# Optimization experiments

Hardware: AMD Instinct MI355X
Metric: run time of the kernel (lower is better)

The kernel has to match this reference:

```python
import math
import jax, jax.numpy as jnp
import numpy as np

EPS = 1e-5

def _ln(x, g, b, axes):
    # LayerNormalization4D / 4DCF: mean/var (unbiased=False) over `axes`
    mu = x.mean(axis=axes, keepdims=True)
    var = ((x - mu) ** 2).mean(axis=axes, keepdims=True)
    return (x - mu) / jnp.sqrt(var + EPS) * g + b

def _prelu(x, a):
    return jnp.where(x >= 0, x, a * x)

def _unfold(x, ks, hs):
    # x: [N, C, Q] -> [N, L, C*ks]; patch layout (c, k) matches F.unfold
    N, C, Qd = x.shape
    L = (Qd - ks) // hs + 1
    idx = jnp.arange(L) * hs
    p = x[:, :, idx[:, None] + jnp.arange(ks)]  # [N, C, L, ks]
    return p.transpose(0, 2, 1, 3).reshape(N, L, C * ks)

def _lstm_dir(xs, Wi, Wh, bi, bh, H):
    # xs: [N, L, Cin]; torch gate order i, f, g, o
    xg = jnp.einsum('nlc,gc->nlg', xs, Wi) + bi + bh  # [N, L, 4H]
    def step(carry, gt):
        h, c = carry
        g = gt + h @ Wh.T
        i, f, gg, o = jnp.split(g, 4, axis=-1)
        c = jax.nn.sigmoid(f) * c + jax.nn.sigmoid(i) * jnp.tanh(gg)
        h = jax.nn.sigmoid(o) * jnp.tanh(c)
        return (h, c), h
    N = xs.shape[0]
    z = jnp.zeros((N, H), xs.dtype)
    _, hs = jax.lax.scan(step, (z, z), jnp.swapaxes(xg, 0, 1))
    return jnp.swapaxes(hs, 0, 1)

def _bilstm(x, wih, whh, bih, bhh):
    H = whh.shape[-1]
    f = _lstm_dir(x, wih[0], whh[0], bih[0], bhh[0], H)
    bk = _lstm_dir(x[:, ::-1], wih[1], whh[1], bih[1], bhh[1], H)[:, ::-1]
    return jnp.concatenate([f, bk], axis=-1)

def _convT1d(x, w, b):
    # x: [N, I, L]; w: [I, O, K] (torch ConvTranspose1d layout); stride 1
    K = w.shape[2]
    w2 = jnp.transpose(w, (1, 0, 2))[:, :, ::-1]
    y = jax.lax.conv_general_dilated(x, w2, (1,), [(K - 1, K - 1)],
                                     dimension_numbers=('NCH', 'OIH', 'NCH'))
    return y + b[None, :, None]

def _forward(x, mouth, intra_g, intra_b, intra_wih, intra_whh, intra_bih, intra_bhh,
             intra_lw, intra_lb, inter_g, inter_b, inter_wih, inter_whh, inter_bih,
             inter_bhh, inter_lw, inter_lb, qw, qb, qa, qg, qbe, kw, kb, ka, kg, kbe,
             vw, vb, va, vg, vbe, pw, pb, pa, pg, pbe):
    emb_ks, emb_hs = 4, 1
    B, C, oT, oQ = x.shape
    T = math.ceil((oT - emb_ks) / emb_hs) * emb_hs + emb_ks
    Qd = math.ceil((oQ - emb_ks) / emb_hs) * emb_hs + emb_ks
    x = jnp.pad(x, ((0, 0), (0, 0), (0, T - oT), (0, Qd - oQ)))
    inp = x
    # ---- intra (biLSTM along freq axis) ----
    h = _ln(inp, intra_g[None, :, None, None], intra_b[None, :, None, None], (1,))
    h = h.transpose(0, 2, 1, 3).reshape(B * T, C, Qd)
    h = _unfold(h, emb_ks, emb_hs)                          # [B*T, L, C*ks]
    h = _bilstm(h, intra_wih, intra_whh, intra_bih, intra_bhh)
    h = _convT1d(h.transpose(0, 2, 1), intra_lw, intra_lb)  # [B*T, C, Qd]
    intra = h.reshape(B, T, C, Qd).transpose(0, 2, 1, 3) + inp
    # ---- inter (biLSTM along time axis) ----
    h = _ln(intra, inter_g[None, :, None, None], inter_b[None, :, None, None], (1,))
    h = h.transpose(0, 3, 1, 2).reshape(B * Qd, C, T)
    h = _unfold(h, emb_ks, emb_hs)
    h = _bilstm(h, inter_wih, inter_whh, inter_bih, inter_bhh)
    h = _convT1d(h.transpose(0, 2, 1), inter_lw, inter_lb)  # [B*Qd, C, T]
    inter = h.reshape(B, Qd, C, T).transpose(0, 2, 3, 1) + intra
    inter = inter[..., :oT, :oQ]                             # [B, C, oT, oQ]
    # ---- multi-head full self-attention over time (conv1x1 QKV per head) ----
    NH = qw.shape[0]
    def qkv(w, b_, a_, g_, be_):
        y = jnp.einsum('bctf,hec->hbetf', inter, w) + b_[:, None, :, None, None]
        y = _prelu(y, a_[:, None, None, None, None])
        return _ln(y, g_[:, None, :, None, :], be_[:, None, :, None, :], (2, 4))
    Qh = qkv(qw, qb, qa, qg, qbe)   # [H, B, E, T, F]
    Kh = qkv(kw, kb, ka, kg, kbe)
    Vh = qkv(vw, vb, va, vg, vbe)   # [H, B, D, T, F]
    E = Qh.shape[2]; D = Vh.shape[2]; F = oQ
    q2 = Qh.transpose(0, 1, 3, 2, 4).reshape(NH, B, oT, E * F)
    k2 = Kh.transpose(0, 1, 3, 2, 4).reshape(NH, B, oT, E * F)
    v2 = Vh.transpose(0, 1, 3, 2, 4).reshape(NH, B, oT, D * F)
    scale = 1.0 / jnp.sqrt(jnp.asarray(E * F, x.dtype))
    attn = jax.nn.softmax(jnp.einsum('hbte,hbse->hbts', q2, k2) * scale, axis=-1)
    o = jnp.einsum('hbts,hbsd->hbtd', attn, v2).reshape(NH, B, oT, D, F)
    o = o.transpose(1, 0, 3, 2, 4).reshape(B, NH * D, oT, F)
    # ---- concat projection ----
    p = jnp.einsum('bctf,oc->botf', o, pw) + pb[None, :, None, None]
    p = _prelu(p, pa)
    p = _ln(p, pg[None, :, None, :], pbe[None, :, None, :], (1, 3))
    return p + inter

def setup_inputs() -> dict:
    key = jax.random.key(0)
    keys = iter(jax.random.split(key, 48))
    f32 = jnp.float32
    def nrm(shape, s=0.05):
        return jax.random.normal(next(keys), shape, f32) * s
    B, C, T, F = 2, 48, 512, 65
    K, H, NH, E = 4, 192, 4, 8
    Cin = C * K
    D = C // NH
    return {
        'x': jax.random.normal(next(keys), (B, C, T, F), f32),
        'mouth': jax.random.normal(next(keys), (B, 64), f32),
        'intra_g': jnp.ones((C,), f32), 'intra_b': jnp.zeros((C,), f32),
        'intra_wih': nrm((2, 4 * H, Cin)), 'intra_whh': nrm((2, 4 * H, H)),
        'intra_bih': nrm((2, 4 * H)), 'intra_bhh': nrm((2, 4 * H)),
        'intra_lw': nrm((2 * H, C, K)), 'intra_lb': nrm((C,)),
        'inter_g': jnp.ones((C,), f32), 'inter_b': jnp.zeros((C,), f32),
        'inter_wih': nrm((2, 4 * H, Cin)), 'inter_whh': nrm((2, 4 * H, H)),
        'inter_bih': nrm((2, 4 * H)), 'inter_bhh': nrm((2, 4 * H)),
        'inter_lw': nrm((2 * H, C, K)), 'inter_lb': nrm((C,)),
        'qw': nrm((NH, E, C)), 'qb': nrm((NH, E)), 'qa': 0.25 * jnp.ones((NH,), f32),
        'qg': jnp.ones((NH, E, F), f32), 'qbe': jnp.zeros((NH, E, F), f32),
        'kw': nrm((NH, E, C)), 'kb': nrm((NH, E)), 'ka': 0.25 * jnp.ones((NH,), f32),
        'kg': jnp.ones((NH, E, F), f32), 'kbe': jnp.zeros((NH, E, F), f32),
        'vw': nrm((NH, D, C)), 'vb': nrm((NH, D)), 'va': 0.25 * jnp.ones((NH,), f32),
        'vg': jnp.ones((NH, D, F), f32), 'vbe': jnp.zeros((NH, D, F), f32),
        'pw': nrm((C, C)), 'pb': nrm((C,)), 'pa': jnp.float32(0.25),
        'pg': jnp.ones((C, F), f32), 'pbe': jnp.zeros((C, F), f32),
    }

def reference(x, mouth, intra_g, intra_b, intra_wih, intra_whh, intra_bih, intra_bhh,
              intra_lw, intra_lb, inter_g, inter_b, inter_wih, inter_whh, inter_bih,
              inter_bhh, inter_lw, inter_lb, qw, qb, qa, qg, qbe, kw, kb, ka, kg, kbe,
              vw, vb, va, vg, vbe, pw, pb, pa, pg, pbe):
    return _forward(x, mouth, intra_g, intra_b, intra_wih, intra_whh, intra_bih,
                    intra_bhh, intra_lw, intra_lb, inter_g, inter_b, inter_wih,
                    inter_whh, inter_bih, inter_bhh, inter_lw, inter_lb, qw, qb, qa,
                    qg, qbe, kw, kb, ka, kg, kbe, vw, vb, va, vg, vbe, pw, pb, pa,
                    pg, pbe)
```

## Files before the change

### kernel.cpp

```cpp
#include <hip/hip_runtime.h>
#include <hip/hip_bf16.h>

typedef __bf16 bf16x8 __attribute__((ext_vector_type(8)));
typedef unsigned short u16x8 __attribute__((ext_vector_type(8)));
typedef float f32x4 __attribute__((ext_vector_type(4)));

#define DEV static __device__ __forceinline__

DEV unsigned short f2bf(float f){
  __hip_bfloat16 h = __float2bfloat16(f);
  return __builtin_bit_cast(unsigned short, h);
}
DEV float b2f(unsigned short u){
  return __bfloat162float(__builtin_bit_cast(__hip_bfloat16, u));
}
DEV float sig2(float xs){
  return __builtin_amdgcn_rcpf(1.0f + __builtin_amdgcn_exp2f(-xs));
}
DEV float tanh2s(float xs){
  return 1.0f - 2.0f*__builtin_amdgcn_rcpf(__builtin_amdgcn_exp2f(xs + xs) + 1.0f);
}
DEV float tanh_n(float x){
  return 1.0f - 2.0f*__builtin_amdgcn_rcpf(__builtin_amdgcn_exp2f(x * 2.885390082f) + 1.0f);
}
DEV void lds_barrier(){
  asm volatile("s_waitcnt lgkmcnt(0)\ns_barrier" ::: "memory");
}


__global__ void zero16(uint4* p, size_t n){
  size_t i = (size_t)blockIdx.x*blockDim.x + threadIdx.x;
  size_t st = (size_t)gridDim.x*blockDim.x;
  uint4 z = make_uint4(0u,0u,0u,0u);
  for (; i < n; i += st) p[i] = z;
}

__global__ void cast_bf(const float* __restrict__ s, unsigned short* __restrict__ d, int n, float scale){
  int i = blockIdx.x*256 + threadIdx.x;
  if (i < n) d[i] = f2bf(s[i]*scale);
}

__global__ void bias_comb(const float* __restrict__ a, const float* __restrict__ b,
                          float* __restrict__ d, int n, float scale){
  int i = blockIdx.x*256 + threadIdx.x;
  if (i < n) d[i] = (a[i] + b[i])*scale;
}

__global__ void lwt_build(const float* __restrict__ lw, unsigned short* __restrict__ lwt){
  int i = blockIdx.x*256 + threadIdx.x;
  if (i < 384*48*4){
    int m = i / 192; int rest = i - m*192; int c = rest >> 2; int k = rest & 3;
    lwt[(size_t)c*1536 + k*384 + m] = f2bf(lw[i]);
  }
}

__global__ __launch_bounds__(256) void ln_unf_intra(
    const float* __restrict__ in, const float* __restrict__ g,
    const float* __restrict__ be, unsigned short* __restrict__ unf)
{
  int bt = blockIdx.x; int b = bt >> 9, t = bt & 511;
  __shared__ float v[48][66];
  __shared__ float mu[65], rs[65];
  __shared__ float g_l[48], b_l[48];
  const float* base = in + (size_t)b*(48*512*65) + (size_t)t*65;
  for (int i = threadIdx.x; i < 48*65; i += 256){
    int c = i/65, q = i - c*65;
    v[c][q] = base[(size_t)c*(512*65) + q];
  }
  if (threadIdx.x < 48){ g_l[threadIdx.x] = g[threadIdx.x]; b_l[threadIdx.x] = be[threadIdx.x]; }
  __syncthreads();
  if (threadIdx.x < 65){
    int q = threadIdx.x; float s=0.f, s2=0.f;
    #pragma unroll
    for (int c = 0; c < 48; c++){ float x = v[c][q]; s += x; s2 += x*x; }
    float m = s*(1.0f/48.0f);
    mu[q] = m; rs[q] = rsqrtf(s2*(1.0f/48.0f) - m*m + 1e-5f);
  }
  __syncthreads();
  unsigned short* orow = unf + (size_t)(b*512 + t)*62*192;
  for (int i = threadIdx.x; i < 62*192; i += 256){
    int l = i/192, j = i - l*192;
    int c = j >> 2, kk = j & 3, q = l + kk;
    float y = (v[c][q]-mu[q])*rs[q]*g_l[c] + b_l[c];
    orow[i] = f2bf(y);
  }
}

__global__ __launch_bounds__(256) void ln_unf_inter(
    const float* __restrict__ in, const float* __restrict__ g,
    const float* __restrict__ be, unsigned short* __restrict__ unf)
{
  int q = blockIdx.x % 65, b = blockIdx.x / 65;
  __shared__ float v[48][132];
  __shared__ float mu[131], rs[131];
  __shared__ float g_l[48], b_l[48];
  if (threadIdx.x < 48){ g_l[threadIdx.x] = g[threadIdx.x]; b_l[threadIdx.x] = be[threadIdx.x]; }
  const float* base = in + (size_t)b*(48*512*65) + q;
  unsigned short* orow = unf + (size_t)(b*65 + q)*509*192;
  for (int t0 = 0; t0 < 512; t0 += 128){
    for (int i = threadIdx.x; i < 48*131; i += 256){
      int c = i/131, tt = i - c*131;
      int t = t0 + tt; t = t > 511 ? 511 : t;
      v[c][tt] = base[((size_t)c*512 + t)*65];
    }
    __syncthreads();
    if (threadIdx.x < 131){
      int tt = threadIdx.x; float s=0.f, s2=0.f;
      #pragma unroll
      for (int c = 0; c < 48; c++){ float x = v[c][tt]; s += x; s2 += x*x; }
      float m = s*(1.0f/48.0f);
      mu[tt] = m; rs[tt] = rsqrtf(s2*(1.0f/48.0f) - m*m + 1e-5f);
    }
    __syncthreads();
    for (int i = threadIdx.x; i < 128*192; i += 256){
      int ll = i/192, j = i - ll*192;
      int l = t0 + ll;
      if (l < 509){
        int c = j >> 2, kk = j & 3, tt = ll + kk;
        float y = (v[c][tt]-mu[tt])*rs[tt]*g_l[c] + b_l[c];
        orow[(size_t)l*192 + j] = f2bf(y);
      }
    }
    __syncthreads();
  }
}

__global__ __launch_bounds__(256) void gemm_xg(
    const unsigned short* __restrict__ unf, const unsigned short* __restrict__ wib,
    const float* __restrict__ bias, unsigned short* __restrict__ xg,
    int NSEQ, int TW, int win0, int L, int nvalid)
{
  const int d = blockIdx.z;
  const int lane = threadIdx.x & 63, wave = threadIdx.x >> 6;
  const int kg = lane >> 4, lr = lane & 15;
  const int nslb = TW >> 3;
  const int sb  = blockIdx.x / nslb;
  const int slb = blockIdx.x - sb*nslb;
  const int nbase = blockIdx.y*64;
  const unsigned short* Bp = wib + (size_t)d*768*192;

  const unsigned short* abase[2];
  #pragma unroll
  for (int mt = 0; mt < 2; mt++){
    int sl = slb*8 + wave*2 + mt;
    int s = win0 + sl;
    int l = d ? (L-1-s) : s;
    l = l < 0 ? 0 : (l > L-1 ? L-1 : l);
    int seq = sb*16 + lr;
    seq = seq < nvalid ? seq : nvalid-1;
    abase[mt] = unf + ((size_t)seq*L + l)*192;
  }

  f32x4 acc[2][4] = {};
  #pragma unroll
  for (int kt = 0; kt < 6; kt++){
    int k0 = kt*32 + kg*8;
    bf16x8 a0 = *(const bf16x8*)(abase[0] + k0);
    bf16x8 a1 = *(const bf16x8*)(abase[1] + k0);
    #pragma unroll
    for (int nt = 0; nt < 4; nt++){
      int n = nbase + nt*16 + lr;
      bf16x8 bfr = *(const bf16x8*)(Bp + (size_t)n*192 + k0);
      acc[0][nt] = __builtin_amdgcn_mfma_f32_16x16x32_bf16(a0, bfr, acc[0][nt], 0,0,0);
      acc[1][nt] = __builtin_amdgcn_mfma_f32_16x16x32_bf16(a1, bfr, acc[1][nt], 0,0,0);
    }
  }
  #pragma unroll
  for (int mt = 0; mt < 2; mt++){
    int sl = slb*8 + wave*2 + mt;
    size_t rowb = (((size_t)d*(NSEQ>>4) + sb)*TW + sl)*768;
    #pragma unroll
    for (int nt = 0; nt < 4; nt++){
      int n = nbase + nt*16 + lr;
      float bs = bias[d*768 + n];
      ushort4 pk;
      pk.x = f2bf(acc[mt][nt][0] + bs);
      pk.y = f2bf(acc[mt][nt][1] + bs);
      pk.z = f2bf(acc[mt][nt][2] + bs);
      pk.w = f2bf(acc[mt][nt][3] + bs);
      *(ushort4*)(xg + (rowb + n)*16 + kg*4) = pk;
    }
  }
}

__global__ __launch_bounds__(768, 3) void lstm_rec(
    const unsigned short* __restrict__ xg,
    const unsigned short* __restrict__ whb,
    unsigned short* __restrict__ hs,
    float* __restrict__ state,
    int NSEQ, int TW, int win0, int L, int Qrows, int nvalid, int steps)
{
  const int d = blockIdx.y;
  const int seq0 = blockIdx.x * 16;
  const int tid = threadIdx.x;
  const int lane = tid & 63, w = tid >> 6;
  const int kg = lane >> 4, lr = lane & 15;
  const int col = w*16 + lr;

  __shared__ unsigned short h_lds[2][16][200];

  bf16x8 whf[4][6];
  #pragma unroll
  for (int g = 0; g < 4; g++){
    const unsigned short* wrow = whb + ((size_t)d*768 + g*192 + col)*192;
    #pragma unroll
    for (int kt = 0; kt < 6; kt++)
      whf[g][kt] = *(const bf16x8*)(wrow + kt*32 + kg*8);
  }

  float c_reg[4];
  unsigned short* hsp[4];
  bool val[4];
  const int l0 = d ? (L-1-win0) : win0;
  const ptrdiff_t ldelta = d ? -384 : 384;
  #pragma unroll
  for (int r = 0; r < 4; r++){
    int m = kg*4 + r;
    const float* st = state + (((size_t)d*NSEQ + seq0 + m)*2)*192;
    h_lds[0][m][col] = f2bf(st[col]);
    c_reg[r] = st[192 + col];
    val[r] = (seq0 + m) < nvalid;
    hsp[r] = hs + ((size_t)(seq0+m)*Qrows + (l0+3))*384 + d*192 + col;
  }
  lds_barrier();

  const unsigned short* xq0 = xg + ((((size_t)d*(NSEQ>>4) + blockIdx.x)*TW)*768)*16
                              + ((size_t)col)*16 + kg*4;
  const size_t SSTR = (size_t)768*16;

  uint2 pfA[4], pfB[4];
  {
    const unsigned short* p1 = xq0 + (steps > 1 ? SSTR : 0);
    #pragma unroll
    for (int g = 0; g < 4; g++){
      pfA[g] = *(const uint2*)(xq0 + (size_t)g*(192*16));
      pfB[g] = *(const uint2*)(p1  + (size_t)g*(192*16));
    }
  }

  int cur = 0;
  auto do_step = [&](uint2 (&pf)[4], int ss){
    f32x4 acc[4];
    #pragma unroll
    for (int g = 0; g < 4; g++){
      unsigned int lo = pf[g].x, hi = pf[g].y;
      acc[g][0] = b2f((unsigned short)(lo & 0xffffu));
      acc[g][1] = b2f((unsigned short)(lo >> 16));
      acc[g][2] = b2f((unsigned short)(hi & 0xffffu));
      acc[g][3] = b2f((unsigned short)(hi >> 16));
    }
    int nss = ss + 2; nss = nss > steps-1 ? steps-1 : nss;
    const unsigned short* np = xq0 + (size_t)nss*SSTR;
    #pragma unroll
    for (int g = 0; g < 4; g++)
      pf[g] = *(const uint2*)(np + (size_t)g*(192*16));
    #pragma unroll
    for (int kt = 0; kt < 6; kt++){
      bf16x8 a = *(const bf16x8*)(&h_lds[cur][lr][kt*32 + kg*8]);
      #pragma unroll
      for (int g = 0; g < 4; g++)
        acc[g] = __builtin_amdgcn_mfma_f32_16x16x32_bf16(a, whf[g][kt], acc[g], 0,0,0);
    }
    #pragma unroll
    for (int r = 0; r < 4; r++){
      float gi = sig2(acc[0][r]);
      float gf = sig2(acc[1][r]);
      float gg = tanh2s(acc[2][r]);
      float go = sig2(acc[3][r]);
      float c = gf*c_reg[r] + gi*gg;
      c_reg[r] = c;
      float h = go*tanh_n(c);
      unsigned short hb = f2bf(h);
      h_lds[cur^1][kg*4 + r][col] = hb;
      if (val[r]) *hsp[r] = hb;
      hsp[r] += ldelta;
    }
    lds_barrier();
    cur ^= 1;
  };

  for (int ss = 0; ss < steps; ss += 2){
    do_step(pfA, ss);
    if (ss + 1 < steps) do_step(pfB, ss + 1);
  }

  #pragma unroll
  for (int r = 0; r < 4; r++){
    int m = kg*4 + r;
    float* st = state + (((size_t)d*NSEQ + seq0 + m)*2)*192;
    st[col] = b2f(h_lds[cur][m][col]);
    st[192 + col] = c_reg[r];
  }
}

__global__ __launch_bounds__(256) void gemm_convt(
    const unsigned short* __restrict__ hs, const unsigned short* __restrict__ lwt,
    const float* __restrict__ lb, const float* __restrict__ addsrc, float* __restrict__ dst,
    int Q, int ddiv, int sA, int sB, int nvalid)
{
  const int lane = threadIdx.x & 63, wave = threadIdx.x >> 6;
  const int kg = lane >> 4, lr = lane & 15;
  const int rowbase = blockIdx.x*128 + wave*32;

  int an[2], aq[2];
  #pragma unroll
  for (int mt = 0; mt < 2; mt++){
    int row = rowbase + mt*16 + lr;
    an[mt] = row / Q; aq[mt] = row - an[mt]*Q;
  }
  f32x4 acc[2][4] = {};
  for (int kt = 0; kt < 48; kt++){
    int k0 = kt*32 + kg*8;
    int tap = k0 / 384;
    int m0 = k0 - tap*384;
    bf16x8 a[2];
    #pragma unroll
    for (int mt = 0; mt < 2; mt++)
      a[mt] = *(const bf16x8*)(hs + ((size_t)an[mt]*(Q+3) + (aq[mt]+3-tap))*384 + m0);
    #pragma unroll
    for (int nt = 0; nt < 4; nt++){
      bf16x8 bfr = *(const bf16x8*)(lwt + (size_t)(nt*16+lr)*1536 + k0);
      acc[0][nt] = __builtin_amdgcn_mfma_f32_16x16x32_bf16(a[0], bfr, acc[0][nt], 0,0,0);
      acc[1][nt] = __builtin_amdgcn_mfma_f32_16x16x32_bf16(a[1], bfr, acc[1][nt], 0,0,0);
    }
  }
  #pragma unroll
  for (int mt = 0; mt < 2; mt++)
  #pragma unroll
  for (int nt = 0; nt < 4; nt++){
    int n = nt*16 + lr;
    if (n >= 48) continue;
    #pragma unroll
    for (int r = 0; r < 4; r++){
      int row = rowbase + mt*16 + kg*4 + r;
      int ns = row / Q, q = row - ns*Q;
      if (ns >= nvalid) continue;
      size_t off = (size_t)(ns/ddiv)*(48*512*65) + (size_t)n*(512*65)
                 + (size_t)(ns % ddiv)*sA + (size_t)q*sB;
      dst[off] = acc[mt][nt][r] + lb[n] + addsrc[off];
    }
  }
}

__global__ __launch_bounds__(256) void gemm_rm(
    const unsigned short* __restrict__ A, const unsigned short* __restrict__ B, float* __restrict__ C,
    int lda, int ldb, int ldc, int KT, int nmax, long long strA, long long strB, long long strC)
{
  const int z = blockIdx.z;
  A += (size_t)z * strA; B += (size_t)z * strB; C += (size_t)z * strC;
  const int lane = threadIdx.x & 63, wave = threadIdx.x >> 6;
  const int kg = lane >> 4, lr = lane & 15;
  const int rowbase = blockIdx.x*128 + wave*32;
  const int nbase = blockIdx.y*64;
  f32x4 acc[2][4] = {};
  for (int kt = 0; kt < KT; kt++){
    int k0 = kt*32 + kg*8;
    bf16x8 a0 = *(const bf16x8*)(A + (size_t)(rowbase+lr)*lda + k0);
    bf16x8 a1 = *(const bf16x8*)(A + (size_t)(rowbase+16+lr)*lda + k0);
    #pragma unroll
    for (int nt = 0; nt < 4; nt++){
      bf16x8 bfr = *(const bf16x8*)(B + (size_t)(nbase+nt*16+lr)*ldb + k0);
      acc[0][nt] = __builtin_amdgcn_mfma_f32_16x16x32_bf16(a0, bfr, acc[0][nt], 0,0,0);
      acc[1][nt] = __builtin_amdgcn_mfma_f32_16x16x32_bf16(a1, bfr, acc[1][nt], 0,0,0);
    }
  }
  #pragma unroll
  for (int mt = 0; mt < 2; mt++)
  #pragma unroll
  for (int nt = 0; nt < 4; nt++)
  #pragma unroll
  for (int r = 0; r < 4; r++){
    int n = nbase + nt*16 + lr;
    if (n < nmax){
      int row = rowbase + mt*16 + kg*4 + r;
      C[(size_t)row*ldc + n] = acc[mt][nt][r];
    }
  }
}

__global__ __launch_bounds__(256) void qkv_k(
    const float* __restrict__ inter, const float* __restrict__ w, const float* __restrict__ bias,
    const float* __restrict__ alpha, const float* __restrict__ gam, const float* __restrict__ bet,
    unsigned short* __restrict__ out, int E, int mode)
{
  int t = blockIdx.x; int hb = blockIdx.y; int h = hb >> 1, b = hb & 1;
  __shared__ float in_l[48][66];
  __shared__ float w_l[12][48];
  __shared__ float y_l[780];
  __shared__ float rs1[4], rs2[4];
  const float* base = inter + (size_t)b*(48*512*65) + (size_t)t*65;
  for (int i = threadIdx.x; i < 48*65; i += 256){
    int c = i/65, f = i - c*65;
    in_l[c][f] = base[(size_t)c*(512*65) + f];
  }
  for (int i = threadIdx.x; i < E*48; i += 256) w_l[i/48][i - (i/48)*48] = w[(size_t)h*E*48 + i];
  __syncthreads();
  int nel = E*65;
  float a = alpha[h];
  float ps = 0.f, pq = 0.f;
  for (int i = threadIdx.x; i < nel; i += 256){
    int e = i/65, f = i - e*65;
    float s = bias[h*E + e];
    #pragma unroll
    for (int c = 0; c < 48; c++) s += w_l[e][c]*in_l[c][f];
    s = s >= 0.f ? s : a*s;
    y_l[i] = s; ps += s; pq += s*s;
  }
  #pragma unroll
  for (int o = 32; o; o >>= 1){ ps += __shfl_xor(ps, o); pq += __shfl_xor(pq, o); }
  if ((threadIdx.x & 63) == 0){ rs1[threadIdx.x>>6] = ps; rs2[threadIdx.x>>6] = pq; }
  __syncthreads();
  ps = rs1[0]+rs1[1]+rs1[2]+rs1[3]; pq = rs2[0]+rs2[1]+rs2[2]+rs2[3];
  float inv = 1.0f/(float)nel;
  float m = ps*inv; float rstd = rsqrtf(pq*inv - m*m + 1e-5f);
  for (int i = threadIdx.x; i < nel; i += 256){
    int e = i/65, f = i - e*65;
    float v = (y_l[i]-m)*rstd*gam[(size_t)(h*E+e)*65 + f] + bet[(size_t)(h*E+e)*65 + f];
    if (mode < 2) out[((size_t)hb*512 + t)*544 + i] = f2bf(v);
    else          out[((size_t)hb*832 + i)*512 + t] = f2bf(v);
  }
}

__global__ __launch_bounds__(256) void softmax_k(const float* __restrict__ S, unsigned short* __restrict__ P){
  size_t row = (size_t)blockIdx.y*512 + blockIdx.x;
  const float* s = S + row*512;
  int tid = threadIdx.x;
  float v0 = s[tid], v1 = s[tid+256];
  float m = fmaxf(v0, v1);
  #pragma unroll
  for (int o = 32; o; o >>= 1) m = fmaxf(m, __shfl_xor(m, o));
  __shared__ float r4[4], q4[4];
  if ((tid & 63) == 0) r4[tid>>6] = m;
  __syncthreads();
  m = fmaxf(fmaxf(r4[0], r4[1]), fmaxf(r4[2], r4[3]));
  const float sc = 0.04385290096535146f;
  float e0 = __expf((v0-m)*sc), e1 = __expf((v1-m)*sc);
  float su = e0 + e1;
  #pragma unroll
  for (int o = 32; o; o >>= 1) su += __shfl_xor(su, o);
  if ((tid & 63) == 0) q4[tid>>6] = su;
  __syncthreads();
  su = q4[0]+q4[1]+q4[2]+q4[3];
  float inv = __builtin_amdgcn_rcpf(su);
  unsigned short* p = P + row*512;
  p[tid] = f2bf(e0*inv); p[tid+256] = f2bf(e1*inv);
}

__global__ __launch_bounds__(256) void pout_k(
    const float* __restrict__ o, const float* __restrict__ pw, const float* __restrict__ pb,
    const float* __restrict__ pa, const float* __restrict__ pg, const float* __restrict__ pbe,
    const float* __restrict__ inter, float* __restrict__ out)
{
  int bt = blockIdx.x; int b = bt >> 9, t = bt & 511;
  __shared__ float o_l[48][66];
  __shared__ float pw_l[48][48];
  __shared__ float p_l[3120];
  __shared__ float rs1[4], rs2[4];
  for (int i = threadIdx.x; i < 48*65; i += 256){
    int c = i/65, f = i - c*65; int h = c/12, dd = c - h*12;
    o_l[c][f] = o[((size_t)(h*2+b)*512 + t)*780 + dd*65 + f];
  }
  for (int i = threadIdx.x; i < 48*48; i += 256) pw_l[i/48][i - (i/48)*48] = pw[i];
  __syncthreads();
  float a = pa[0];
  float ps = 0.f, pq = 0.f;
  for (int i = threadIdx.x; i < 3120; i += 256){
    int oc = i/65, f = i - oc*65;
    float s = pb[oc];
    #pragma unroll
    for (int c = 0; c < 48; c++) s += pw_l[oc][c]*o_l[c][f];
    s = s >= 0.f ? s : a*s;
    p_l[i] = s; ps += s; pq += s*s;
  }
  #pragma unroll
  for (int o2 = 32; o2; o2 >>= 1){ ps += __shfl_xor(ps, o2); pq += __shfl_xor(pq, o2); }
  if ((threadIdx.x & 63) == 0){ rs1[threadIdx.x>>6] = ps; rs2[threadIdx.x>>6] = pq; }
  __syncthreads();
  ps = rs1[0]+rs1[1]+rs1[2]+rs1[3]; pq = rs2[0]+rs2[1]+rs2[2]+rs2[3];
  float m = ps*(1.0f/3120.0f); float rstd = rsqrtf(pq*(1.0f/3120.0f) - m*m + 1e-5f);
  for (int i = threadIdx.x; i < 3120; i += 256){
    int oc = i/65, f = i - oc*65;
    size_t off = ((size_t)(b*48+oc)*512 + t)*65 + f;
    out[off] = (p_l[i]-m)*rstd*pg[i] + pbe[i] + inter[off];
  }
}


extern "C" void kernel_launch(void* const* d_in, const int* in_sizes, int n_in,
                              void* d_out, int out_size, void* d_ws, size_t ws_size,
                              hipStream_t stream)
{
  const float* x         = (const float*)d_in[0];
  const float* intra_g   = (const float*)d_in[2];
  const float* intra_b   = (const float*)d_in[3];
  const float* intra_wih = (const float*)d_in[4];
  const float* intra_whh = (const float*)d_in[5];
  const float* intra_bih = (const float*)d_in[6];
  const float* intra_bhh = (const float*)d_in[7];
  const float* intra_lw  = (const float*)d_in[8];
  const float* intra_lb  = (const float*)d_in[9];
  const float* inter_g   = (const float*)d_in[10];
  const float* inter_b   = (const float*)d_in[11];
  const float* inter_wih = (const float*)d_in[12];
  const float* inter_whh = (const float*)d_in[13];
  const float* inter_bih = (const float*)d_in[14];
  const float* inter_bhh = (const float*)d_in[15];
  const float* inter_lw  = (const float*)d_in[16];
  const float* inter_lb  = (const float*)d_in[17];
  const float* qw  = (const float*)d_in[18];
  const float* qb  = (const float*)d_in[19];
  const float* qa  = (const float*)d_in[20];
  const float* qg  = (const float*)d_in[21];
  const float* qbe = (const float*)d_in[22];
  const float* kw  = (const float*)d_in[23];
  const float* kb  = (const float*)d_in[24];
  const float* ka  = (const float*)d_in[25];
  const float* kgm = (const float*)d_in[26];
  const float* kbe = (const float*)d_in[27];
  const float* vw  = (const float*)d_in[28];
  const float* vb  = (const float*)d_in[29];
  const float* va  = (const float*)d_in[30];
  const float* vg  = (const float*)d_in[31];
  const float* vbe = (const float*)d_in[32];
  const float* pw  = (const float*)d_in[33];
  const float* pb  = (const float*)d_in[34];
  const float* pa  = (const float*)d_in[35];
  const float* pgm = (const float*)d_in[36];
  const float* pbe = (const float*)d_in[37];

  char* ws = (char*)d_ws;
  constexpr size_t WIB_INTRA = 0;
  constexpr size_t WHB_INTRA = 589824;
  constexpr size_t WIB_INTER = 1179648;
  constexpr size_t WHB_INTER = 1769472;
  constexpr size_t LWT_INTRA = 2359296;
  constexpr size_t LWT_INTER = 2555904;
  constexpr size_t BIAS_INTRA = 2752512;
  constexpr size_t BIAS_INTER = 2758656;
  constexpr size_t UNF   = 2764800;
  constexpr size_t INTER = 2764800;
  constexpr size_t STATE = 28311552;
  constexpr size_t HS    = 31457280;
  constexpr size_t INTRA = 84934656;
  constexpr size_t XG    = 97714176;
  constexpr size_t Q2B   = XG;
  constexpr size_t K2B   = XG + 4456448;
  constexpr size_t V2T   = XG + 8912896;
  constexpr size_t SCORES= XG + 15728640;
  constexpr size_t ATTNB = XG + 24117248;
  constexpr size_t OBUF  = XG + 28311552;

  auto U16 = [&](size_t off){ return (unsigned short*)(ws + off); };
  auto F32 = [&](size_t off){ return (float*)(ws + off); };

  const float LOG2E = 1.4426950408889634f;

  zero16<<<512,256,0,stream>>>((uint4*)(ws+LWT_INTRA), 393216/16);
  cast_bf<<<1152,256,0,stream>>>(intra_wih, U16(WIB_INTRA), 294912, LOG2E);
  cast_bf<<<1152,256,0,stream>>>(intra_whh, U16(WHB_INTRA), 294912, LOG2E);
  cast_bf<<<1152,256,0,stream>>>(inter_wih, U16(WIB_INTER), 294912, LOG2E);
  cast_bf<<<1152,256,0,stream>>>(inter_whh, U16(WHB_INTER), 294912, LOG2E);
  bias_comb<<<6,256,0,stream>>>(intra_bih, intra_bhh, F32(BIAS_INTRA), 1536, LOG2E);
  bias_comb<<<6,256,0,stream>>>(inter_bih, inter_bhh, F32(BIAS_INTER), 1536, LOG2E);
  lwt_build<<<288,256,0,stream>>>(intra_lw, U16(LWT_INTRA));
  lwt_build<<<288,256,0,stream>>>(inter_lw, U16(LWT_INTER));

  ln_unf_intra<<<1024,256,0,stream>>>(x, intra_g, intra_b, U16(UNF));
  zero16<<<2048,256,0,stream>>>((uint4*)(ws+HS), 53477376/16);
  zero16<<<2048,256,0,stream>>>((uint4*)(ws+STATE), 3145728/16);
  for (int w = 0; w < 4; w++){
    int win0 = w*16;
    int steps = (62 - win0) < 16 ? (62 - win0) : 16;
    gemm_xg<<<dim3(128,12,2),256,0,stream>>>(U16(UNF), U16(WIB_INTRA), F32(BIAS_INTRA), U16(XG),
                                             1024, 16, win0, 62, 1024);
    lstm_rec<<<dim3(64,2),768,0,stream>>>(U16(XG), U16(WHB_INTRA), U16(HS), F32(STATE),
                                          1024, 16, win0, 62, 68, 1024, steps);
  }
  gemm_convt<<<dim3(520,1),256,0,stream>>>(U16(HS), U16(LWT_INTRA), intra_lb, x, F32(INTRA),
                                           65, 512, 65, 1, 1024);

  ln_unf_inter<<<130,256,0,stream>>>(F32(INTRA), inter_g, inter_b, U16(UNF));
  zero16<<<2048,256,0,stream>>>((uint4*)(ws+HS), 51417600/16);
  zero16<<<2048,256,0,stream>>>((uint4*)(ws+STATE), 3145728/16);
  for (int w = 0; w < 8; w++){
    int win0 = w*64;
    int steps = (509 - win0) < 64 ? (509 - win0) : 64;
    gemm_xg<<<dim3(72,12,2),256,0,stream>>>(U16(UNF), U16(WIB_INTER), F32(BIAS_INTER), U16(XG),
                                            144, 64, win0, 509, 130);
    lstm_rec<<<dim3(9,2),768,0,stream>>>(U16(XG), U16(WHB_INTER), U16(HS), F32(STATE),
                                         144, 64, win0, 509, 515, 130, steps);
  }
  gemm_convt<<<dim3(576,1),256,0,stream>>>(U16(HS), U16(LWT_INTER), inter_lb, F32(INTRA), F32(INTER),
                                           512, 65, 1, 65, 130);

  zero16<<<2048,256,0,stream>>>((uint4*)(ws+Q2B), 15728640/16);
  qkv_k<<<dim3(512,8),256,0,stream>>>(F32(INTER), qw, qb, qa, qg, qbe, U16(Q2B), 8, 0);
  qkv_k<<<dim3(512,8),256,0,stream>>>(F32(INTER), kw, kb, ka, kgm, kbe, U16(K2B), 8, 1);
  qkv_k<<<dim3(512,8),256,0,stream>>>(F32(INTER), vw, vb, va, vg, vbe, U16(V2T), 12, 2);
  gemm_rm<<<dim3(4,8,8),256,0,stream>>>(U16(Q2B), U16(K2B), F32(SCORES),
                                        544, 544, 512, 17, 512,
                                        (long long)512*544, (long long)512*544, (long long)512*512);
  softmax_k<<<dim3(512,8),256,0,stream>>>(F32(SCORES), U16(ATTNB));
  gemm_rm<<<dim3(4,13,8),256,0,stream>>>(U16(ATTNB), U16(V2T), F32(OBUF),
                                         512, 512, 780, 16, 780,
                                         (long long)512*512, (long long)832*512, (long long)512*780);
  pout_k<<<1024,256,0,stream>>>(F32(OBUF), pw, pb, pa, pgm, pbe, F32(INTER), (float*)d_out);
}
```

Before: 1.979 ms.

## Reorder unfold layout to tap-major and tile convT GEMM through LDS

Reorders the unfolded-input feature layout from (c,k) to (k,c) and permutes the input-projection weights to match, so the LN/unfold kernels can write vectorized 8-element bf16 chunks. The inter-path LN/unfold now runs one block per (b,t) row, scattering into up to four unfold rows, which gives far more blocks than the old per-q kernel. The convT GEMM is templated per mode, stages its overlapping hidden-state window in LDS for reuse across taps, and in intra mode writes float4 coalesced outputs through an LDS transpose. The costs are larger LDS use per block and many scattered small stores in the inter unfold.

New measurement: 1.960 ms. About the same (-1.0%).

```diff
diff --git a/kernel.cpp b/kernel.cpp
--- a/kernel.cpp
+++ b/kernel.cpp
@@ -38,6 +38,15 @@
 __global__ void cast_bf(const float* __restrict__ s, unsigned short* __restrict__ d, int n, float scale){
   int i = blockIdx.x*256 + threadIdx.x;
   if (i < n) d[i] = f2bf(s[i]*scale);
+}
+
+__global__ void cast_wi(const float* __restrict__ s, unsigned short* __restrict__ d, float scale){
+  int i = blockIdx.x*256 + threadIdx.x;
+  if (i < 294912){
+    int dn = i/192, k = i - dn*192;
+    int c = k >> 2, kk = k & 3;
+    d[(size_t)dn*192 + kk*48 + c] = f2bf(s[i]*scale);
+  }
 }
 
 __global__ void bias_comb(const float* __restrict__ a, const float* __restrict__ b,
@@ -78,11 +87,22 @@
   }
   __syncthreads();
   unsigned short* orow = unf + (size_t)(b*512 + t)*62*192;
-  for (int i = threadIdx.x; i < 62*192; i += 256){
-    int l = i/192, j = i - l*192;
-    int c = j >> 2, kk = j & 3, q = l + kk;
-    float y = (v[c][q]-mu[q])*rs[q]*g_l[c] + b_l[c];
-    orow[i] = f2bf(y);
+  for (int idx = threadIdx.x; idx < 62*24; idx += 256){
+    int l = idx/24, jg = idx - l*24;
+    int kk = jg/6, c0 = (jg - kk*6)*8;
+    int q = l + kk;
+    ushort4 p0, p1;
+    float mq = mu[q], rq = rs[q];
+    p0.x = f2bf((v[c0+0][q]-mq)*rq*g_l[c0+0] + b_l[c0+0]);
+    p0.y = f2bf((v[c0+1][q]-mq)*rq*g_l[c0+1] + b_l[c0+1]);
+    p0.z = f2bf((v[c0+2][q]-mq)*rq*g_l[c0+2] + b_l[c0+2]);
+    p0.w = f2bf((v[c0+3][q]-mq)*rq*g_l[c0+3] + b_l[c0+3]);
+    p1.x = f2bf((v[c0+4][q]-mq)*rq*g_l[c0+4] + b_l[c0+4]);
+    p1.y = f2bf((v[c0+5][q]-mq)*rq*g_l[c0+5] + b_l[c0+5]);
+    p1.z = f2bf((v[c0+6][q]-mq)*rq*g_l[c0+6] + b_l[c0+6]);
+    p1.w = f2bf((v[c0+7][q]-mq)*rq*g_l[c0+7] + b_l[c0+7]);
+    *(ushort4*)(orow + (size_t)l*192 + kk*48 + c0) = p0;
+    *(ushort4*)(orow + (size_t)l*192 + kk*48 + c0 + 4) = p1;
   }
 }
 
@@ -90,38 +110,44 @@
     const float* __restrict__ in, const float* __restrict__ g,
     const float* __restrict__ be, unsigned short* __restrict__ unf)
 {
-  int q = blockIdx.x % 65, b = blockIdx.x / 65;
-  __shared__ float v[48][132];
-  __shared__ float mu[131], rs[131];
+  int bt = blockIdx.x; int b = bt >> 9, t = bt & 511;
+  __shared__ float v[48][66];
+  __shared__ float mu[65], rs[65];
   __shared__ float g_l[48], b_l[48];
+  const float* base = in + (size_t)b*(48*512*65) + (size_t)t*65;
+  for (int i = threadIdx.x; i < 48*65; i += 256){
+    int c = i/65, q = i - c*65;
+    v[c][q] = base[(size_t)c*(512*65) + q];
+  }
   if (threadIdx.x < 48){ g_l[threadIdx.x] = g[threadIdx.x]; b_l[threadIdx.x] = be[threadIdx.x]; }
-  const float* base = in + (size_t)b*(48*512*65) + q;
-  unsigned short* orow = unf + (size_t)(b*65 + q)*509*192;
-  for (int t0 = 0; t0 < 512; t0 += 128){
-    for (int i = threadIdx.x; i < 48*131; i += 256){
-      int c = i/131, tt = i - c*131;
-      int t = t0 + tt; t = t > 511 ? 511 : t;
-      v[c][tt] = base[((size_t)c*512 + t)*65];
-    }
-    __syncthreads();
-    if (threadIdx.x < 131){
-      int tt = threadIdx.x; float s=0.f, s2=0.f;
-      #pragma unroll
-      for (int c = 0; c < 48; c++){ float x = v[c][tt]; s += x; s2 += x*x; }
-      float m = s*(1.0f/48.0f);
-      mu[tt] = m; rs[tt] = rsqrtf(s2*(1.0f/48.0f) - m*m + 1e-5f);
-    }
-    __syncthreads();
-    for (int i = threadIdx.x; i < 128*192; i += 256){
-      int ll = i/192, j = i - ll*192;
-      int l = t0 + ll;
-      if (l < 509){
-        int c = j >> 2, kk = j & 3, tt = ll + kk;
-        float y = (v[c][tt]-mu[tt])*rs[tt]*g_l[c] + b_l[c];
-        orow[(size_t)l*192 + j] = f2bf(y);
-      }
-    }
-    __syncthreads();
+  __syncthreads();
+  if (threadIdx.x < 65){
+    int q = threadIdx.x; float s=0.f, s2=0.f;
+    #pragma unroll
+    for (int c = 0; c < 48; c++){ float x = v[c][q]; s += x; s2 += x*x; }
+    float m = s*(1.0f/48.0f);
+    mu[q] = m; rs[q] = rsqrtf(s2*(1.0f/48.0f) - m*m + 1e-5f);
+  }
+  __syncthreads();
+  for (int idx = threadIdx.x; idx < 4*65*6; idx += 256){
+    int s = idx/390;
+    int rem = idx - s*390;
+    int q = rem/6, c0 = (rem - q*6)*8;
+    int l = t - 3 + s, kk = 3 - s;
+    if (l < 0 || l > 508) continue;
+    float mq = mu[q], rq = rs[q];
+    ushort4 p0, p1;
+    p0.x = f2bf((v[c0+0][q]-mq)*rq*g_l[c0+0] + b_l[c0+0]);
+    p0.y = f2bf((v[c0+1][q]-mq)*rq*g_l[c0+1] + b_l[c0+1]);
+    p0.z = f2bf((v[c0+2][q]-mq)*rq*g_l[c0+2] + b_l[c0+2]);
+    p0.w = f2bf((v[c0+3][q]-mq)*rq*g_l[c0+3] + b_l[c0+3]);
+    p1.x = f2bf((v[c0+4][q]-mq)*rq*g_l[c0+4] + b_l[c0+4]);
+    p1.y = f2bf((v[c0+5][q]-mq)*rq*g_l[c0+5] + b_l[c0+5]);
+    p1.z = f2bf((v[c0+6][q]-mq)*rq*g_l[c0+6] + b_l[c0+6]);
+    p1.w = f2bf((v[c0+7][q]-mq)*rq*g_l[c0+7] + b_l[c0+7]);
+    size_t addr = ((size_t)(b*65+q)*509 + l)*192 + kk*48 + c0;
+    *(ushort4*)(unf + addr) = p0;
+    *(ushort4*)(unf + addr + 4) = p1;
   }
 }
 
@@ -293,51 +319,80 @@
   }
 }
 
+template<int MODE>
 __global__ __launch_bounds__(256) void gemm_convt(
     const unsigned short* __restrict__ hs, const unsigned short* __restrict__ lwt,
-    const float* __restrict__ lb, const float* __restrict__ addsrc, float* __restrict__ dst,
-    int Q, int ddiv, int sA, int sB, int nvalid)
-{
+    const float* __restrict__ lb, const float* __restrict__ addsrc, float* __restrict__ dst)
+{
+  constexpr int Q  = MODE ? 512 : 65;
   const int lane = threadIdx.x & 63, wave = threadIdx.x >> 6;
   const int kg = lane >> 4, lr = lane & 15;
-  const int rowbase = blockIdx.x*128 + wave*32;
-
-  int an[2], aq[2];
-  #pragma unroll
-  for (int mt = 0; mt < 2; mt++){
-    int row = rowbase + mt*16 + lr;
-    an[mt] = row / Q; aq[mt] = row - an[mt]*Q;
-  }
-  f32x4 acc[2][4] = {};
+  const int R0 = blockIdx.x * 64;
+
+  __shared__ union U {
+    unsigned short a[70][392];
+    float c[64][52];
+  } sm;
+
+  const int HB0 = R0 + 3*(R0/Q);
+  for (int idx = threadIdx.x; idx < 70*48; idx += 256){
+    int j = idx/48, seg = idx - j*48;
+    *(uint4*)&sm.a[j][seg*8] = *(const uint4*)(hs + ((size_t)(HB0+j))*384 + seg*8);
+  }
+  __syncthreads();
+
+  const int row = R0 + wave*16 + lr;
+  const int an = row / Q;
+  const int jb = row + 3*an - HB0;
+
+  f32x4 acc[4] = {};
   for (int kt = 0; kt < 48; kt++){
     int k0 = kt*32 + kg*8;
     int tap = k0 / 384;
     int m0 = k0 - tap*384;
-    bf16x8 a[2];
-    #pragma unroll
-    for (int mt = 0; mt < 2; mt++)
-      a[mt] = *(const bf16x8*)(hs + ((size_t)an[mt]*(Q+3) + (aq[mt]+3-tap))*384 + m0);
+    bf16x8 a = *(const bf16x8*)(&sm.a[jb + 3 - tap][m0]);
     #pragma unroll
     for (int nt = 0; nt < 4; nt++){
       bf16x8 bfr = *(const bf16x8*)(lwt + (size_t)(nt*16+lr)*1536 + k0);
-      acc[0][nt] = __builtin_amdgcn_mfma_f32_16x16x32_bf16(a[0], bfr, acc[0][nt], 0,0,0);
-      acc[1][nt] = __builtin_amdgcn_mfma_f32_16x16x32_bf16(a[1], bfr, acc[1][nt], 0,0,0);
-    }
-  }
-  #pragma unroll
-  for (int mt = 0; mt < 2; mt++)
-  #pragma unroll
-  for (int nt = 0; nt < 4; nt++){
-    int n = nt*16 + lr;
-    if (n >= 48) continue;
-    #pragma unroll
-    for (int r = 0; r < 4; r++){
-      int row = rowbase + mt*16 + kg*4 + r;
-      int ns = row / Q, q = row - ns*Q;
-      if (ns >= nvalid) continue;
-      size_t off = (size_t)(ns/ddiv)*(48*512*65) + (size_t)n*(512*65)
-                 + (size_t)(ns % ddiv)*sA + (size_t)q*sB;
-      dst[off] = acc[mt][nt][r] + lb[n] + addsrc[off];
+      acc[nt] = __builtin_amdgcn_mfma_f32_16x16x32_bf16(a, bfr, acc[nt], 0,0,0);
+    }
+  }
+
+  if (MODE == 0){
+    __syncthreads();
+    #pragma unroll
+    for (int nt = 0; nt < 3; nt++)
+      #pragma unroll
+      for (int r = 0; r < 4; r++)
+        sm.c[wave*16 + kg*4 + r][nt*16 + lr] = acc[nt][r];
+    __syncthreads();
+    const int b = R0 >= 33280 ? 1 : 0;
+    const size_t bb = (size_t)b*1597440;
+    const int rb = R0 - b*33280;
+    for (int idx = threadIdx.x; idx < 48*16; idx += 256){
+      int n = idx >> 4, g = idx & 15;
+      size_t off = bb + (size_t)n*33280 + rb + g*4;
+      float4 av = *(const float4*)(addsrc + off);
+      float lbn = lb[n];
+      float4 o;
+      o.x = sm.c[g*4+0][n] + lbn + av.x;
+      o.y = sm.c[g*4+1][n] + lbn + av.y;
+      o.z = sm.c[g*4+2][n] + lbn + av.z;
+      o.w = sm.c[g*4+3][n] + lbn + av.w;
+      *(float4*)(dst + off) = o;
+    }
+  } else {
+    #pragma unroll
+    for (int nt = 0; nt < 3; nt++){
+      int n = nt*16 + lr;
+      float lbn = lb[n];
+      #pragma unroll
+      for (int r = 0; r < 4; r++){
+        int orow = R0 + wave*16 + kg*4 + r;
+        int ns = orow >> 9, t = orow & 511;
+        size_t off = (size_t)(ns/65)*1597440 + (size_t)n*33280 + (ns%65) + (size_t)t*65;
+        dst[off] = acc[nt][r] + lbn + addsrc[off];
+      }
     }
   }
 }
@@ -556,9 +611,9 @@
   const float LOG2E = 1.4426950408889634f;
 
   zero16<<<512,256,0,stream>>>((uint4*)(ws+LWT_INTRA), 393216/16);
-  cast_bf<<<1152,256,0,stream>>>(intra_wih, U16(WIB_INTRA), 294912, LOG2E);
+  cast_wi<<<1152,256,0,stream>>>(intra_wih, U16(WIB_INTRA), LOG2E);
   cast_bf<<<1152,256,0,stream>>>(intra_whh, U16(WHB_INTRA), 294912, LOG2E);
-  cast_bf<<<1152,256,0,stream>>>(inter_wih, U16(WIB_INTER), 294912, LOG2E);
+  cast_wi<<<1152,256,0,stream>>>(inter_wih, U16(WIB_INTER), LOG2E);
   cast_bf<<<1152,256,0,stream>>>(inter_whh, U16(WHB_INTER), 294912, LOG2E);
   bias_comb<<<6,256,0,stream>>>(intra_bih, intra_bhh, F32(BIAS_INTRA), 1536, LOG2E);
   bias_comb<<<6,256,0,stream>>>(inter_bih, inter_bhh, F32(BIAS_INTER), 1536, LOG2E);
@@ -576,10 +631,9 @@
     lstm_rec<<<dim3(64,2),768,0,stream>>>(U16(XG), U16(WHB_INTRA), U16(HS), F32(STATE),
                                           1024, 16, win0, 62, 68, 1024, steps);
   }
-  gemm_convt<<<dim3(520,1),256,0,stream>>>(U16(HS), U16(LWT_INTRA), intra_lb, x, F32(INTRA),
-                                           65, 512, 65, 1, 1024);
-
-  ln_unf_inter<<<130,256,0,stream>>>(F32(INTRA), inter_g, inter_b, U16(UNF));
+  gemm_convt<0><<<1040,256,0,stream>>>(U16(HS), U16(LWT_INTRA), intra_lb, x, F32(INTRA));
+
+  ln_unf_inter<<<1024,256,0,stream>>>(F32(INTRA), inter_g, inter_b, U16(UNF));
   zero16<<<2048,256,0,stream>>>((uint4*)(ws+HS), 51417600/16);
   zero16<<<2048,256,0,stream>>>((uint4*)(ws+STATE), 3145728/16);
   for (int w = 0; w < 8; w++){
@@ -590,8 +644,7 @@
     lstm_rec<<<dim3(9,2),768,0,stream>>>(U16(XG), U16(WHB_INTER), U16(HS), F32(STATE),
                                          144, 64, win0, 509, 515, 130, steps);
   }
-  gemm_convt<<<dim3(576,1),256,0,stream>>>(U16(HS), U16(LWT_INTER), inter_lb, F32(INTRA), F32(INTER),
-                                           512, 65, 1, 65, 130);
+  gemm_convt<1><<<1040,256,0,stream>>>(U16(HS), U16(LWT_INTER), inter_lb, F32(INTRA), F32(INTER));
 
   zero16<<<2048,256,0,stream>>>((uint4*)(ws+Q2B), 15728640/16);
   qkv_k<<<dim3(512,8),256,0,stream>>>(F32(INTER), qw, qb, qa, qg, qbe, U16(Q2B), 8, 0);
```
